# Performance work log

Measured on AMD Instinct MI355X. Metric: run time of the kernel, lower is better.

The kernel has to match this reference:

```python
import jax, jax.numpy as jnp
import numpy as np

N = 30000      # nodes
E = 480000     # edges (before self loops)
C = 64         # in_channels
L = 32         # latent_dim
H = 2          # heads
SLOPE = 0.2    # PyG GATConv default negative_slope


def _param(key, shape, fan_in):
    return jax.random.normal(key, shape, jnp.float32) * (1.0 / np.sqrt(fan_in))


def setup_inputs() -> dict:
    key = jax.random.key(0)
    ks = jax.random.split(key, 32)
    d = {
        "x": jax.random.normal(ks[0], (N, C), jnp.float32),
        "edge_index": jax.random.randint(ks[1], (2, E), 0, N),
        "use_neighbors": 1,
        # GATConv params: W [heads*out, in], att_src/att_dst [heads, out], bias [heads*out]
        # encoder_conv1: in=C, out=2C, heads=H
        "W1": _param(ks[2], (H * 2 * C, C), C),
        "as1": _param(ks[3], (H, 2 * C), 2 * C),
        "ad1": _param(ks[4], (H, 2 * C), 2 * C),
        "b1": jnp.zeros((H * 2 * C,), jnp.float32),
        # encoder_conv2: in=2C*H, out=L, heads=1
        "W2": _param(ks[5], (L, 2 * C * H), 2 * C * H),
        "as2": _param(ks[6], (1, L), L),
        "ad2": _param(ks[7], (1, L), L),
        "b2": jnp.zeros((L,), jnp.float32),
        # decoder_conv1: in=L, out=2C, heads=H
        "W3": _param(ks[8], (H * 2 * C, L), L),
        "as3": _param(ks[9], (H, 2 * C), 2 * C),
        "ad3": _param(ks[10], (H, 2 * C), 2 * C),
        "b3": jnp.zeros((H * 2 * C,), jnp.float32),
        # decoder_conv2: in=2C*H, out=C, heads=1
        "W4": _param(ks[11], (C, 2 * C * H), 2 * C * H),
        "as4": _param(ks[12], (1, C), C),
        "ad4": _param(ks[13], (1, C), C),
        "b4": jnp.zeros((C,), jnp.float32),
        # dense (non-neighbor) branch Linear params [out, in] + bias
        "el1w": _param(ks[14], (2 * C, C), C), "el1b": jnp.zeros((2 * C,), jnp.float32),
        "el2w": _param(ks[15], (L, 2 * C), 2 * C), "el2b": jnp.zeros((L,), jnp.float32),
        "dl1w": _param(ks[16], (2 * C, L), L), "dl1b": jnp.zeros((2 * C,), jnp.float32),
        "dl2w": _param(ks[17], (C, 2 * C), 2 * C), "dl2b": jnp.zeros((C,), jnp.float32),
    }
    return d


def gat_conv(x, src, dst, W, att_src, att_dst, bias, heads, out_ch):
    """PyG GATConv (concat=True, self loops already in src/dst)."""
    n = x.shape[0]
    h = (x @ W.T).reshape(n, heads, out_ch)            # [N,H,F]
    a_s = jnp.sum(h * att_src[None], -1)               # [N,H]
    a_d = jnp.sum(h * att_dst[None], -1)               # [N,H]
    e = jax.nn.leaky_relu(a_s[src] + a_d[dst], SLOPE)  # [Etot,H]
    m = jax.ops.segment_max(e, dst, num_segments=n)
    ex = jnp.exp(e - m[dst])
    den = jax.ops.segment_sum(ex, dst, num_segments=n)
    alpha = ex / den[dst]                              # segment softmax over incoming edges
    msg = h[src] * alpha[..., None]                    # [Etot,H,F]
    out = jax.ops.segment_sum(msg, dst, num_segments=n)
    return out.reshape(n, heads * out_ch) + bias


def reference(x, edge_index, use_neighbors,
              W1, as1, ad1, b1, W2, as2, ad2, b2,
              W3, as3, ad3, b3, W4, as4, ad4, b4,
              el1w, el1b, el2w, el2b, dl1w, dl1b, dl2w, dl2b):
    if use_neighbors:
        loops = jnp.arange(N)
        src = jnp.concatenate([edge_index[0], loops])
        dst = jnp.concatenate([edge_index[1], loops])
        h = jax.nn.relu(gat_conv(x, src, dst, W1, as1, ad1, b1, H, 2 * C))
        z = gat_conv(h, src, dst, W2, as2, ad2, b2, 1, L)
        h = jax.nn.relu(gat_conv(z, src, dst, W3, as3, ad3, b3, H, 2 * C))
        return gat_conv(h, src, dst, W4, as4, ad4, b4, 1, C)
    else:
        h = jax.nn.relu(x @ el1w.T + el1b)
        z = h @ el2w.T + el2b
        h = jax.nn.relu(z @ dl1w.T + dl1b)
        return h @ dl2w.T + dl2b
```

## Files before the change

### kernel.cpp

```cpp
#include <hip/hip_runtime.h>
#include <hip/hip_bf16.h>
#include <math.h>

#define NODES 30000
#define WAVE 64
#define SCAN_T 1024
#define SCAN_CH 32
#define SCAN_CAP (SCAN_T * SCAN_CH)

typedef __attribute__((ext_vector_type(8))) short short8b;
typedef __attribute__((ext_vector_type(4))) float floatx4;

static __device__ __forceinline__ float lrelu(float x) {
    return (x > 0.f) ? x : 0.2f * x;
}

static __device__ __forceinline__ unsigned short f2bf(float f) {
    union { float f; unsigned u; } v; v.f = f;
    unsigned r = v.u + 0x7FFF + ((v.u >> 16) & 1);
    return (unsigned short)(r >> 16);
}

static __device__ __forceinline__ void unpack8(uint4 q, float* v) {
    v[0] = __uint_as_float(q.x << 16); v[1] = __uint_as_float(q.x & 0xFFFF0000u);
    v[2] = __uint_as_float(q.y << 16); v[3] = __uint_as_float(q.y & 0xFFFF0000u);
    v[4] = __uint_as_float(q.z << 16); v[5] = __uint_as_float(q.z & 0xFFFF0000u);
    v[6] = __uint_as_float(q.w << 16); v[7] = __uint_as_float(q.w & 0xFFFF0000u);
}

static __device__ __forceinline__ uint4 pack8(const float* v) {
    uint4 p;
    p.x = (unsigned)f2bf(v[0]) | ((unsigned)f2bf(v[1]) << 16);
    p.y = (unsigned)f2bf(v[2]) | ((unsigned)f2bf(v[3]) << 16);
    p.z = (unsigned)f2bf(v[4]) | ((unsigned)f2bf(v[5]) << 16);
    p.w = (unsigned)f2bf(v[6]) | ((unsigned)f2bf(v[7]) << 16);
    return p;
}

__global__ __launch_bounds__(256) void prep(
    int* __restrict__ deg,
    float* __restrict__ z0, float* __restrict__ z1,
    float* __restrict__ z2, float* __restrict__ z3,
    const float* __restrict__ W1, unsigned short* __restrict__ wb1,
    const float* __restrict__ W2, unsigned short* __restrict__ wb2,
    const float* __restrict__ W3, unsigned short* __restrict__ wb3,
    const float* __restrict__ W4, unsigned short* __restrict__ wb4,
    const float* __restrict__ x, unsigned short* __restrict__ xb,
    const int* __restrict__ flag)
{
    if (*flag == 0) return;
    const int tid = blockIdx.x * blockDim.x + threadIdx.x;
    const int stride = gridDim.x * blockDim.x;
    for (int i = tid; i < SCAN_CAP / 4; i += stride)
        reinterpret_cast<int4*>(deg)[i] = make_int4(0, 0, 0, 0);
    for (int i = tid; i < NODES; i += stride) {
        z0[i] = 0.f; z1[i] = 0.f; z2[i] = 0.f; z3[i] = 0.f;
    }
    for (int i = tid; i < 256 * 64; i += stride) wb1[i] = f2bf(W1[i]);
    for (int i = tid; i < 32 * 256; i += stride) wb2[i] = f2bf(W2[i]);
    for (int i = tid; i < 256 * 32; i += stride) wb3[i] = f2bf(W3[i]);
    for (int i = tid; i < 64 * 256; i += stride) wb4[i] = f2bf(W4[i]);
    for (int i = tid; i < NODES * 64 / 4; i += stride) {
        float4 v = reinterpret_cast<const float4*>(x)[i];
        ushort4 o;
        o.x = f2bf(v.x); o.y = f2bf(v.y); o.z = f2bf(v.z); o.w = f2bf(v.w);
        reinterpret_cast<ushort4*>(xb)[i] = o;
    }
}

template <int K, int M, int OUT_BF16, int RELU, int DOTS>
__global__ __launch_bounds__(256) void gemm_mfma(
    const unsigned short* __restrict__ Xb, int ldx,
    const unsigned short* __restrict__ Wb,
    const float* __restrict__ bias,
    void* __restrict__ outv, int ldc,
    const float* __restrict__ att_s, const float* __restrict__ att_d,
    float* __restrict__ as_out, float* __restrict__ ad_out,
    const int* __restrict__ flag, int Nrows)
{
    if (*flag == 0) return;
    constexpr int KC = K / 32;
    const int w    = threadIdx.x >> 6;
    const int lane = threadIdx.x & 63;
    const int z    = blockIdx.z;
    const int ct   = blockIdx.y;
    const int rowBase = blockIdx.x * 64 + w * 16;

    const int lr = lane & 15;
    const int lk = (lane >> 4) * 8;

    const int arow = min(rowBase + lr, Nrows - 1);
    const unsigned short* ap = Xb + (size_t)arow * ldx + z * K + lk;
    short8b a[KC];
#pragma unroll
    for (int kc = 0; kc < KC; kc++)
        a[kc] = *reinterpret_cast<const short8b*>(ap + kc * 32);

    const unsigned short* bp = Wb + (size_t)(z * M + ct * 16 + lr) * K + lk;
    short8b b[KC];
#pragma unroll
    for (int kc = 0; kc < KC; kc++)
        b[kc] = *reinterpret_cast<const short8b*>(bp + kc * 32);

    floatx4 c = {0.f, 0.f, 0.f, 0.f};
#pragma unroll
    for (int kc = 0; kc < KC; kc++)
        c = __builtin_amdgcn_mfma_f32_16x16x32_bf16(a[kc], b[kc], c, 0, 0, 0);

    const int colg = z * M + ct * 16 + lr;
    const float bv = bias ? bias[colg] : 0.f;

#pragma unroll
    for (int i = 0; i < 4; i++) {
        int r = rowBase + (lane >> 4) * 4 + i;
        float v = c[i] + bv;
        if (RELU) v = fmaxf(v, 0.f);
        if (r < Nrows) {
            if (OUT_BF16)
                ((unsigned short*)outv)[(size_t)r * ldc + colg] = f2bf(v);
            else
                ((float*)outv)[(size_t)r * ldc + colg] = v;
        }
    }

    if (DOTS) {
        const float as_v = att_s[colg];
        const float ad_v = att_d[colg];
#pragma unroll
        for (int i = 0; i < 4; i++) {
            int r = rowBase + (lane >> 4) * 4 + i;
            float ps = c[i] * as_v;
            float pd = c[i] * ad_v;
#pragma unroll
            for (int off = 8; off; off >>= 1) {
                ps += __shfl_xor(ps, off);
                pd += __shfl_xor(pd, off);
            }
            if (lr == 0 && r < Nrows) {
                atomicAdd(&as_out[r], ps);
                atomicAdd(&ad_out[r], pd);
            }
        }
    }
}

__global__ __launch_bounds__(256) void gemm_xwt(
    const float* __restrict__ X, int lda, const float* __restrict__ W,
    const float* __restrict__ bias, float* __restrict__ out, int ldc,
    int Nrows, int M, int K, int relu,
    const int* __restrict__ flag, int wantFlag)
{
    if (((*flag != 0) ? 1 : 0) != wantFlag) return;

    const int z = blockIdx.z;
    X += (size_t)z * K;
    W += (size_t)z * M * K;
    if (bias) bias += (size_t)z * M;
    out += (size_t)z * M;

    __shared__ float As[16][68];
    __shared__ float Bs[16][68];

    const int t  = threadIdx.x;
    const int tx = t & 15;
    const int ty = t >> 4;
    const int rowBase = blockIdx.y * 64;
    const int colBase = blockIdx.x * 64;

    float acc[4][4];
#pragma unroll
    for (int i = 0; i < 4; i++)
#pragma unroll
        for (int j = 0; j < 4; j++) acc[i][j] = 0.f;

    const int r_ld = t >> 2;
    const int k_ld = (t & 3) * 4;

    for (int kt = 0; kt < K; kt += 16) {
        float4 av = make_float4(0.f, 0.f, 0.f, 0.f);
        int grow = rowBase + r_ld;
        if (grow < Nrows)
            av = *reinterpret_cast<const float4*>(&X[(size_t)grow * lda + kt + k_ld]);
        As[k_ld + 0][r_ld] = av.x;
        As[k_ld + 1][r_ld] = av.y;
        As[k_ld + 2][r_ld] = av.z;
        As[k_ld + 3][r_ld] = av.w;
        float4 bv = make_float4(0.f, 0.f, 0.f, 0.f);
        int gm = colBase + r_ld;
        if (gm < M)
            bv = *reinterpret_cast<const float4*>(&W[(size_t)gm * K + kt + k_ld]);
        Bs[k_ld + 0][r_ld] = bv.x;
        Bs[k_ld + 1][r_ld] = bv.y;
        Bs[k_ld + 2][r_ld] = bv.z;
        Bs[k_ld + 3][r_ld] = bv.w;
        __syncthreads();

#pragma unroll
        for (int kk = 0; kk < 16; ++kk) {
            const float4 a = *reinterpret_cast<const float4*>(&As[kk][ty * 4]);
            const float4 b = *reinterpret_cast<const float4*>(&Bs[kk][tx * 4]);
            acc[0][0] += a.x * b.x; acc[0][1] += a.x * b.y; acc[0][2] += a.x * b.z; acc[0][3] += a.x * b.w;
            acc[1][0] += a.y * b.x; acc[1][1] += a.y * b.y; acc[1][2] += a.y * b.z; acc[1][3] += a.y * b.w;
            acc[2][0] += a.z * b.x; acc[2][1] += a.z * b.y; acc[2][2] += a.z * b.z; acc[2][3] += a.z * b.w;
            acc[3][0] += a.w * b.x; acc[3][1] += a.w * b.y; acc[3][2] += a.w * b.z; acc[3][3] += a.w * b.w;
        }
        __syncthreads();
    }

#pragma unroll
    for (int i = 0; i < 4; i++) {
        int row = rowBase + ty * 4 + i;
        if (row >= Nrows) continue;
        int col0 = colBase + tx * 4;
        if (col0 >= M) continue;
        float4 v = make_float4(acc[i][0], acc[i][1], acc[i][2], acc[i][3]);
        if (bias) {
            v.x += bias[col0 + 0]; v.y += bias[col0 + 1];
            v.z += bias[col0 + 2]; v.w += bias[col0 + 3];
        }
        if (relu) {
            v.x = fmaxf(v.x, 0.f); v.y = fmaxf(v.y, 0.f);
            v.z = fmaxf(v.z, 0.f); v.w = fmaxf(v.w, 0.f);
        }
        *reinterpret_cast<float4*>(&out[(size_t)row * ldc + col0]) = v;
    }
}

template <int HH, int F, int K>
static __device__ void fold_body(
    const float* __restrict__ W, const float* __restrict__ as_,
    const float* __restrict__ ad_, float* __restrict__ us,
    float* __restrict__ ud, int b)
{
    const int sel = b / HH;
    const int h   = b % HH;
    const float* att = sel ? ad_ : as_;
    float* uo = sel ? ud : us;

    constexpr int NG = 256 / K;
    const int k  = threadIdx.x % K;
    const int fg = threadIdx.x / K;

    float s = 0.f;
#pragma unroll
    for (int f = fg; f < F; f += NG)
        s += att[h * F + f] * W[(size_t)(h * F + f) * K + k];

    __shared__ float red[256];
    red[threadIdx.x] = s;
    __syncthreads();
    if (fg == 0) {
        float tot = s;
#pragma unroll
        for (int g = 1; g < NG; g++) tot += red[g * K + k];
        uo[h * K + k] = tot;
    }
}

__global__ __launch_bounds__(256) void fold_att2(
    const float* __restrict__ W1, const float* __restrict__ as1,
    const float* __restrict__ ad1, float* __restrict__ u1s, float* __restrict__ u1d,
    const float* __restrict__ W3, const float* __restrict__ as3,
    const float* __restrict__ ad3, float* __restrict__ u3s, float* __restrict__ u3d,
    const int* __restrict__ flag)
{
    if (*flag == 0) return;
    const int b = blockIdx.x;
    if (b < 4) fold_body<2, 128, 64>(W1, as1, ad1, u1s, u1d, b);
    else       fold_body<2, 128, 32>(W3, as3, ad3, u3s, u3d, b - 4);
}

template <int K, int HH>
__global__ __launch_bounds__(256) void att_from_x(
    const float* __restrict__ xin, const float* __restrict__ us,
    const float* __restrict__ ud, float* __restrict__ as_out,
    float* __restrict__ ad_out, const int* __restrict__ flag)
{
    if (*flag == 0) return;
    constexpr int NPW = WAVE / K;
    const int wid  = threadIdx.x >> 6;
    const int lane = threadIdx.x & 63;
    const int sub  = lane / K;
    const int col  = lane % K;
    const int node = (blockIdx.x * 4 + wid) * NPW + sub;

    float v = 0.f;
    if (node < NODES) v = xin[(size_t)node * K + col];
    float ps[HH], pd[HH];
#pragma unroll
    for (int h = 0; h < HH; h++) {
        ps[h] = v * us[h * K + col];
        pd[h] = v * ud[h * K + col];
    }
#pragma unroll
    for (int off = K / 2; off; off >>= 1) {
#pragma unroll
        for (int h = 0; h < HH; h++) {
            ps[h] += __shfl_xor(ps[h], off);
            pd[h] += __shfl_xor(pd[h], off);
        }
    }
    if (col == 0 && node < NODES) {
#pragma unroll
        for (int h = 0; h < HH; h++) {
            as_out[node * HH + h] = ps[h];
            ad_out[node * HH + h] = pd[h];
        }
    }
}

template <int K, int HH>
__global__ __launch_bounds__(256) void gat_aggr_x(
    const unsigned short* __restrict__ xb, const float* __restrict__ as_,
    const float* __restrict__ ad_, const int* __restrict__ rowptr,
    const int* __restrict__ csr_src, unsigned short* __restrict__ aggb,
    const int* __restrict__ flag)
{
    if (*flag == 0) return;
    const int node = blockIdx.x * 4 + (threadIdx.x >> 6);
    const int lane = threadIdx.x & 63;
    if (node >= NODES) return;

    const int beg = rowptr[node], end = rowptr[node + 1];
    const int deg = end - beg;

    float adv[HH];
#pragma unroll
    for (int h = 0; h < HH; h++) adv[h] = ad_[node * HH + h];

    float wl[HH];
    float mx[HH], rden[HH];
    int s_l = 0;
    const bool fast = (deg <= WAVE);

    if (fast) {
        float e[HH];
        int i = beg + lane;
        if (i < end) {
            s_l = csr_src[i];
#pragma unroll
            for (int h = 0; h < HH; h++)
                e[h] = lrelu(as_[s_l * HH + h] + adv[h]);
        } else {
#pragma unroll
            for (int h = 0; h < HH; h++) e[h] = -1e30f;
        }
#pragma unroll
        for (int h = 0; h < HH; h++) {
            mx[h] = e[h];
#pragma unroll
            for (int off = 32; off; off >>= 1)
                mx[h] = fmaxf(mx[h], __shfl_xor(mx[h], off));
            float ex = __expf(e[h] - mx[h]);
            wl[h] = ex;
            float dn = ex;
#pragma unroll
            for (int off = 32; off; off >>= 1)
                dn += __shfl_xor(dn, off);
            rden[h] = 1.f / dn;
        }
    } else {
        float den[HH];
#pragma unroll
        for (int h = 0; h < HH; h++) { mx[h] = -1e30f; den[h] = 0.f; }
        for (int i = beg + lane; i < end; i += WAVE) {
            int s = csr_src[i];
#pragma unroll
            for (int h = 0; h < HH; h++)
                mx[h] = fmaxf(mx[h], lrelu(as_[s * HH + h] + adv[h]));
        }
#pragma unroll
        for (int h = 0; h < HH; h++)
#pragma unroll
            for (int off = 32; off; off >>= 1)
                mx[h] = fmaxf(mx[h], __shfl_xor(mx[h], off));
        for (int i = beg + lane; i < end; i += WAVE) {
            int s = csr_src[i];
#pragma unroll
            for (int h = 0; h < HH; h++)
                den[h] += __expf(lrelu(as_[s * HH + h] + adv[h]) - mx[h]);
        }
#pragma unroll
        for (int h = 0; h < HH; h++) {
#pragma unroll
            for (int off = 32; off; off >>= 1)
                den[h] += __shfl_xor(den[h], off);
            rden[h] = 1.f / den[h];
        }
    }

    constexpr int LPG = K / 8;
    constexpr int GR  = WAVE / LPG;
    const int esub = lane / LPG;
    const int c8   = lane % LPG;

    float acc[HH][8];
#pragma unroll
    for (int h = 0; h < HH; h++)
#pragma unroll
        for (int j = 0; j < 8; j++) acc[h][j] = 0.f;

    if (fast) {
        const int iters = (deg + GR - 1) / GR;
        for (int it = 0; it < iters; ++it) {
            const int i = beg + it * GR + esub;
            const bool valid = (i < end);
            const int srcl = valid ? (i - beg) : 0;
            int s = __shfl(s_l, srcl);
            float w[HH];
#pragma unroll
            for (int h = 0; h < HH; h++)
                w[h] = __shfl(wl[h], srcl);
            if (valid) {
                uint4 q = *reinterpret_cast<const uint4*>(&xb[(size_t)s * K + c8 * 8]);
                float v[8];
                unpack8(q, v);
#pragma unroll
                for (int h = 0; h < HH; h++)
#pragma unroll
                    for (int j = 0; j < 8; j++)
                        acc[h][j] += v[j] * w[h];
            }
        }
    } else {
        for (int i = beg + esub; i < end; i += GR) {
            int s = csr_src[i];
            float w[HH];
#pragma unroll
            for (int h = 0; h < HH; h++)
                w[h] = __expf(lrelu(as_[s * HH + h] + adv[h]) - mx[h]);
            uint4 q = *reinterpret_cast<const uint4*>(&xb[(size_t)s * K + c8 * 8]);
            float v[8];
            unpack8(q, v);
#pragma unroll
            for (int h = 0; h < HH; h++)
#pragma unroll
                for (int j = 0; j < 8; j++)
                    acc[h][j] += v[j] * w[h];
        }
    }
#pragma unroll
    for (int off = LPG; off < WAVE; off <<= 1)
#pragma unroll
        for (int h = 0; h < HH; h++)
#pragma unroll
            for (int j = 0; j < 8; j++)
                acc[h][j] += __shfl_xor(acc[h][j], off);

    if (esub == 0) {
#pragma unroll
        for (int h = 0; h < HH; h++) {
            float o[8];
#pragma unroll
            for (int j = 0; j < 8; j++) o[j] = acc[h][j] * rden[h];
            *reinterpret_cast<uint4*>(&aggb[(size_t)node * (HH * K) + h * K + c8 * 8]) = pack8(o);
        }
    }
}

template <int HF, int RELU, int OUTB>
__global__ __launch_bounds__(256) void gat_aggr_h(
    const unsigned short* __restrict__ hb, const float* __restrict__ as_,
    const float* __restrict__ ad_, const int* __restrict__ rowptr,
    const int* __restrict__ csr_src, const float* __restrict__ bias,
    float* __restrict__ out, unsigned short* __restrict__ outb,
    const int* __restrict__ flag)
{
    if (*flag == 0) return;
    const int node = blockIdx.x * 4 + (threadIdx.x >> 6);
    const int lane = threadIdx.x & 63;
    if (node >= NODES) return;

    const int beg = rowptr[node], end = rowptr[node + 1];
    const int deg = end - beg;
    const float adv = ad_[node];

    float wl, mx, rden;
    int s_l = 0;
    const bool fast = (deg <= WAVE);

    if (fast) {
        int i = beg + lane;
        float e = -1e30f;
        if (i < end) {
            s_l = csr_src[i];
            e = lrelu(as_[s_l] + adv);
        }
        mx = e;
#pragma unroll
        for (int off = 32; off; off >>= 1)
            mx = fmaxf(mx, __shfl_xor(mx, off));
        wl = __expf(e - mx);
        float dn = wl;
#pragma unroll
        for (int off = 32; off; off >>= 1)
            dn += __shfl_xor(dn, off);
        rden = 1.f / dn;
    } else {
        mx = -1e30f;
        float den = 0.f;
        for (int i = beg + lane; i < end; i += WAVE) {
            int s = csr_src[i];
            mx = fmaxf(mx, lrelu(as_[s] + adv));
        }
#pragma unroll
        for (int off = 32; off; off >>= 1)
            mx = fmaxf(mx, __shfl_xor(mx, off));
        for (int i = beg + lane; i < end; i += WAVE) {
            int s = csr_src[i];
            den += __expf(lrelu(as_[s] + adv) - mx);
        }
#pragma unroll
        for (int off = 32; off; off >>= 1)
            den += __shfl_xor(den, off);
        rden = 1.f / den;
        wl = 0.f;
    }

    constexpr int LPG = HF / 8;
    constexpr int GR  = WAVE / LPG;
    const int esub = lane / LPG;
    const int c8   = lane % LPG;

    float acc[8];
#pragma unroll
    for (int j = 0; j < 8; j++) acc[j] = 0.f;

    if (fast) {
        const int iters = (deg + GR - 1) / GR;
        for (int it = 0; it < iters; ++it) {
            const int i = beg + it * GR + esub;
            const bool valid = (i < end);
            const int srcl = valid ? (i - beg) : 0;
            int s = __shfl(s_l, srcl);
            float w = __shfl(wl, srcl);
            if (valid) {
                uint4 q = *reinterpret_cast<const uint4*>(&hb[(size_t)s * HF + c8 * 8]);
                float v[8];
                unpack8(q, v);
#pragma unroll
                for (int j = 0; j < 8; j++) acc[j] += v[j] * w;
            }
        }
    } else {
        for (int i = beg + esub; i < end; i += GR) {
            int s = csr_src[i];
            float w = __expf(lrelu(as_[s] + adv) - mx);
            uint4 q = *reinterpret_cast<const uint4*>(&hb[(size_t)s * HF + c8 * 8]);
            float v[8];
            unpack8(q, v);
#pragma unroll
            for (int j = 0; j < 8; j++) acc[j] += v[j] * w;
        }
    }
#pragma unroll
    for (int off = LPG; off < WAVE; off <<= 1)
#pragma unroll
        for (int j = 0; j < 8; j++)
            acc[j] += __shfl_xor(acc[j], off);

    if (esub == 0) {
        const int col0 = c8 * 8;
        float o[8];
#pragma unroll
        for (int j = 0; j < 8; j++) {
            o[j] = acc[j] * rden + bias[col0 + j];
            if (RELU) o[j] = fmaxf(o[j], 0.f);
        }
        float4 o0 = make_float4(o[0], o[1], o[2], o[3]);
        float4 o1 = make_float4(o[4], o[5], o[6], o[7]);
        *reinterpret_cast<float4*>(&out[(size_t)node * HF + col0]) = o0;
        *reinterpret_cast<float4*>(&out[(size_t)node * HF + col0 + 4]) = o1;
        if (OUTB)
            *reinterpret_cast<uint4*>(&outb[(size_t)node * HF + col0]) = pack8(o);
    }
}

__global__ void count_deg(const int* __restrict__ ei, int* __restrict__ deg,
                          int E_, int Nn, const int* __restrict__ flag)
{
    if (*flag == 0) return;
    int e = blockIdx.x * blockDim.x + threadIdx.x;
    int tot = E_ + Nn;
    if (e >= tot) return;
    int dst = (e < E_) ? ei[E_ + e] : (e - E_);
    atomicAdd(&deg[dst], 1);
}

__global__ __launch_bounds__(SCAN_T) void scan_deg(
    const int* __restrict__ deg, int* __restrict__ rowptr,
    int* __restrict__ cursor, const int* __restrict__ flag)
{
    if (*flag == 0) return;
    __shared__ int sums[SCAN_T];
    const int t = threadIdx.x;
    const int base = t * SCAN_CH;

    int v[SCAN_CH];
    const int4* dp = reinterpret_cast<const int4*>(deg + base);
#pragma unroll
    for (int j = 0; j < SCAN_CH / 4; j++) {
        int4 q = dp[j];
        v[4 * j + 0] = q.x; v[4 * j + 1] = q.y;
        v[4 * j + 2] = q.z; v[4 * j + 3] = q.w;
    }
    int s = 0;
#pragma unroll
    for (int j = 0; j < SCAN_CH; j++) s += v[j];
    sums[t] = s;
    __syncthreads();
    for (int off = 1; off < SCAN_T; off <<= 1) {
        int x = (t >= off) ? sums[t - off] : 0;
        __syncthreads();
        sums[t] += x;
        __syncthreads();
    }
    int run = sums[t] - s;
    if (t == 0) rowptr[0] = 0;
#pragma unroll
    for (int j = 0; j < SCAN_CH; j++) {
        cursor[base + j] = run;
        run += v[j];
        rowptr[base + j + 1] = run;
    }
}

__global__ void scatter_edges(const int* __restrict__ ei, int* __restrict__ cursor,
                              int* __restrict__ csr_src, int E_, int Nn,
                              const int* __restrict__ flag)
{
    if (*flag == 0) return;
    int e = blockIdx.x * blockDim.x + threadIdx.x;
    int tot = E_ + Nn;
    if (e >= tot) return;
    int src, dst;
    if (e < E_) { src = ei[e]; dst = ei[E_ + e]; }
    else        { src = e - E_; dst = src; }
    int pos = atomicAdd(&cursor[dst], 1);
    csr_src[pos] = src;
}

extern "C" void kernel_launch(void* const* d_in, const int* in_sizes, int n_in,
                              void* d_out, int out_size, void* d_ws, size_t ws_size,
                              hipStream_t stream)
{
    const float* x    = (const float*)d_in[0];
    const int*   ei   = (const int*)d_in[1];
    const int*   flag = (const int*)d_in[2];
    const float* W1 = (const float*)d_in[3];
    const float* as1 = (const float*)d_in[4];
    const float* ad1 = (const float*)d_in[5];
    const float* b1 = (const float*)d_in[6];
    const float* W2 = (const float*)d_in[7];
    const float* as2 = (const float*)d_in[8];
    const float* ad2 = (const float*)d_in[9];
    const float* b2 = (const float*)d_in[10];
    const float* W3 = (const float*)d_in[11];
    const float* as3 = (const float*)d_in[12];
    const float* ad3 = (const float*)d_in[13];
    const float* b3 = (const float*)d_in[14];
    const float* W4 = (const float*)d_in[15];
    const float* as4 = (const float*)d_in[16];
    const float* ad4 = (const float*)d_in[17];
    const float* b4 = (const float*)d_in[18];
    const float* el1w = (const float*)d_in[19];
    const float* el1b = (const float*)d_in[20];
    const float* el2w = (const float*)d_in[21];
    const float* el2b = (const float*)d_in[22];
    const float* dl1w = (const float*)d_in[23];
    const float* dl1b = (const float*)d_in[24];
    const float* dl2w = (const float*)d_in[25];
    const float* dl2b = (const float*)d_in[26];

    const int E_   = in_sizes[1] / 2;
    const int Etot = E_ + NODES;

    char* base = (char*)d_ws;
    size_t off = 0;
    auto carve = [&](size_t bytes) -> void* {
        void* p = base + off;
        off = (off + bytes + 255) & ~(size_t)255;
        return p;
    };
    float* T0  = (float*)carve((size_t)NODES * 128 * 4);
    float* A   = (float*)carve((size_t)NODES * 256 * 4);
    float* Bz  = (float*)carve((size_t)NODES * 32 * 4);
    float* asb = (float*)carve((size_t)NODES * 2 * 4);
    float* adb = (float*)carve((size_t)NODES * 2 * 4);
    float* as2b = (float*)carve((size_t)NODES * 4);
    float* ad2b = (float*)carve((size_t)NODES * 4);
    float* as4b = (float*)carve((size_t)NODES * 4);
    float* ad4b = (float*)carve((size_t)NODES * 4);
    float* u1s = (float*)carve(2 * 64 * 4);
    float* u1d = (float*)carve(2 * 64 * 4);
    float* u3s = (float*)carve(2 * 32 * 4);
    float* u3d = (float*)carve(2 * 32 * 4);
    unsigned short* xb   = (unsigned short*)carve((size_t)NODES * 64 * 2);
    unsigned short* aggb = (unsigned short*)carve((size_t)NODES * 128 * 2);
    unsigned short* Ab   = (unsigned short*)carve((size_t)NODES * 256 * 2);
    unsigned short* T1b  = (unsigned short*)carve((size_t)NODES * 64 * 2);
    unsigned short* Bzb  = (unsigned short*)carve((size_t)NODES * 32 * 2);
    unsigned short* wb1  = (unsigned short*)carve(256 * 64 * 2);
    unsigned short* wb2  = (unsigned short*)carve(32 * 256 * 2);
    unsigned short* wb3  = (unsigned short*)carve(256 * 32 * 2);
    unsigned short* wb4  = (unsigned short*)carve(64 * 256 * 2);
    int* deg    = (int*)carve((size_t)SCAN_CAP * 4);
    int* rowptr = (int*)carve((size_t)(SCAN_CAP + 1) * 4);
    int* cursor = (int*)carve((size_t)SCAN_CAP * 4);
    int* csr    = (int*)carve((size_t)Etot * 4);
    (void)ws_size; (void)n_in; (void)out_size;

    float* outp = (float*)d_out;

    const int nodeBlocks = (NODES + 3) / 4;
    const int edgeBlocks = (Etot + 255) / 256;
    dim3 blk(256);
    const int rowTiles = (NODES + 63) / 64;

    prep<<<2048, 256, 0, stream>>>(deg, as2b, ad2b, as4b, ad4b,
                                   W1, wb1, W2, wb2, W3, wb3, W4, wb4,
                                   x, xb, flag);
    count_deg<<<edgeBlocks, 256, 0, stream>>>(ei, deg, E_, NODES, flag);
    scan_deg<<<1, SCAN_T, 0, stream>>>(deg, rowptr, cursor, flag);
    scatter_edges<<<edgeBlocks, 256, 0, stream>>>(ei, cursor, csr, E_, NODES, flag);

    fold_att2<<<8, 256, 0, stream>>>(W1, as1, ad1, u1s, u1d,
                                     W3, as3, ad3, u3s, u3d, flag);

    att_from_x<64, 2><<<nodeBlocks, blk, 0, stream>>>(x, u1s, u1d, asb, adb, flag);
    gat_aggr_x<64, 2><<<nodeBlocks, blk, 0, stream>>>(xb, asb, adb, rowptr, csr, aggb, flag);
    gemm_mfma<64, 128, 1, 1, 0><<<dim3(rowTiles, 8, 2), blk, 0, stream>>>(
        aggb, 128, wb1, b1, Ab, 256, nullptr, nullptr, nullptr, nullptr, flag, NODES);

    gemm_mfma<256, 32, 1, 0, 1><<<dim3(rowTiles, 2, 1), blk, 0, stream>>>(
        Ab, 256, wb2, nullptr, T1b, 32, as2, ad2, as2b, ad2b, flag, NODES);
    gat_aggr_h<32, 0, 1><<<nodeBlocks, blk, 0, stream>>>(T1b, as2b, ad2b, rowptr, csr, b2, Bz, Bzb, flag);

    att_from_x<32, 2><<<(NODES + 7) / 8, blk, 0, stream>>>(Bz, u3s, u3d, asb, adb, flag);
    gat_aggr_x<32, 2><<<nodeBlocks, blk, 0, stream>>>(Bzb, asb, adb, rowptr, csr, aggb, flag);
    gemm_mfma<32, 128, 1, 1, 0><<<dim3(rowTiles, 8, 2), blk, 0, stream>>>(
        aggb, 64, wb3, b3, Ab, 256, nullptr, nullptr, nullptr, nullptr, flag, NODES);

    gemm_mfma<256, 64, 1, 0, 1><<<dim3(rowTiles, 4, 1), blk, 0, stream>>>(
        Ab, 256, wb4, nullptr, T1b, 64, as4, ad4, as4b, ad4b, flag, NODES);
    gat_aggr_h<64, 0, 0><<<nodeBlocks, blk, 0, stream>>>(T1b, as4b, ad4b, rowptr, csr, b4, outp, nullptr, flag);

    gemm_xwt<<<dim3(2, rowTiles, 1), blk, 0, stream>>>(x,  64,  el1w, el1b, T0,   128, NODES, 128, 64, 1, flag, 0);
    gemm_xwt<<<dim3(1, rowTiles, 1), blk, 0, stream>>>(T0, 128, el2w, el2b, Bz,   32,  NODES, 32, 128, 0, flag, 0);
    gemm_xwt<<<dim3(2, rowTiles, 1), blk, 0, stream>>>(Bz, 32,  dl1w, dl1b, A,    128, NODES, 128, 32, 1, flag, 0);
    gemm_xwt<<<dim3(1, rowTiles, 1), blk, 0, stream>>>(A,  128, dl2w, dl2b, outp, 64,  NODES, 64, 128, 0, flag, 0);
}
```

Measured before the change: 382.1 us.

## Fuse preprocessing kernels to cut launches in GAT pipeline

Degree counting and the attention-weight folding move into the prep kernel, and the degree buffer is now zeroed with hipMemsetAsync. Edge scatter and the first-layer attention dot products run as one combined launch. The third layer's attention logits are computed inside the second aggregation kernel's epilogue. This removes several small kernel launches and one full pass over Bz, in exchange for more complex kernels and a memset call.

```diff
diff --git a/kernel.cpp b/kernel.cpp
--- a/kernel.cpp
+++ b/kernel.cpp
@@ -37,8 +37,38 @@
     return p;
 }
 
-__global__ __launch_bounds__(256) void prep(
-    int* __restrict__ deg,
+template <int HH, int F, int K>
+static __device__ void fold_body(
+    const float* __restrict__ W, const float* __restrict__ as_,
+    const float* __restrict__ ad_, float* __restrict__ us,
+    float* __restrict__ ud, int b, float* red)
+{
+    const int sel = b / HH;
+    const int h   = b % HH;
+    const float* att = sel ? ad_ : as_;
+    float* uo = sel ? ud : us;
+
+    constexpr int NG = 256 / K;
+    const int k  = threadIdx.x % K;
+    const int fg = threadIdx.x / K;
+
+    float s = 0.f;
+#pragma unroll
+    for (int f = fg; f < F; f += NG)
+        s += att[h * F + f] * W[(size_t)(h * F + f) * K + k];
+
+    red[threadIdx.x] = s;
+    __syncthreads();
+    if (fg == 0) {
+        float tot = s;
+#pragma unroll
+        for (int g = 1; g < NG; g++) tot += red[g * K + k];
+        uo[h * K + k] = tot;
+    }
+}
+
+__global__ __launch_bounds__(256) void prep2(
+    const int* __restrict__ ei, int E_, int* __restrict__ deg,
     float* __restrict__ z0, float* __restrict__ z1,
     float* __restrict__ z2, float* __restrict__ z3,
     const float* __restrict__ W1, unsigned short* __restrict__ wb1,
@@ -46,13 +76,22 @@
     const float* __restrict__ W3, unsigned short* __restrict__ wb3,
     const float* __restrict__ W4, unsigned short* __restrict__ wb4,
     const float* __restrict__ x, unsigned short* __restrict__ xb,
+    const float* __restrict__ as1, const float* __restrict__ ad1,
+    float* __restrict__ u1s, float* __restrict__ u1d,
+    const float* __restrict__ as3, const float* __restrict__ ad3,
+    float* __restrict__ u3s, float* __restrict__ u3d,
     const int* __restrict__ flag)
 {
     if (*flag == 0) return;
+    __shared__ float red[256];
     const int tid = blockIdx.x * blockDim.x + threadIdx.x;
     const int stride = gridDim.x * blockDim.x;
-    for (int i = tid; i < SCAN_CAP / 4; i += stride)
-        reinterpret_cast<int4*>(deg)[i] = make_int4(0, 0, 0, 0);
+
+    const int tot = E_ + NODES;
+    for (int e = tid; e < tot; e += stride) {
+        int dst = (e < E_) ? ei[E_ + e] : (e - E_);
+        atomicAdd(&deg[dst], 1);
+    }
     for (int i = tid; i < NODES; i += stride) {
         z0[i] = 0.f; z1[i] = 0.f; z2[i] = 0.f; z3[i] = 0.f;
     }
@@ -65,6 +104,100 @@
         ushort4 o;
         o.x = f2bf(v.x); o.y = f2bf(v.y); o.z = f2bf(v.z); o.w = f2bf(v.w);
         reinterpret_cast<ushort4*>(xb)[i] = o;
+    }
+
+    if (blockIdx.x < 8) {
+        __syncthreads();
+        if (blockIdx.x < 4)
+            fold_body<2, 128, 64>(W1, as1, ad1, u1s, u1d, blockIdx.x, red);
+        else
+            fold_body<2, 128, 32>(W3, as3, ad3, u3s, u3d, blockIdx.x - 4, red);
+    }
+}
+
+__global__ __launch_bounds__(SCAN_T) void scan_deg(
+    const int* __restrict__ deg, int* __restrict__ rowptr,
+    int* __restrict__ cursor, const int* __restrict__ flag)
+{
+    if (*flag == 0) return;
+    __shared__ int sums[SCAN_T];
+    const int t = threadIdx.x;
+    const int base = t * SCAN_CH;
+
+    int v[SCAN_CH];
+    const int4* dp = reinterpret_cast<const int4*>(deg + base);
+#pragma unroll
+    for (int j = 0; j < SCAN_CH / 4; j++) {
+        int4 q = dp[j];
+        v[4 * j + 0] = q.x; v[4 * j + 1] = q.y;
+        v[4 * j + 2] = q.z; v[4 * j + 3] = q.w;
+    }
+    int s = 0;
+#pragma unroll
+    for (int j = 0; j < SCAN_CH; j++) s += v[j];
+    sums[t] = s;
+    __syncthreads();
+    for (int off = 1; off < SCAN_T; off <<= 1) {
+        int x = (t >= off) ? sums[t - off] : 0;
+        __syncthreads();
+        sums[t] += x;
+        __syncthreads();
+    }
+    int run = sums[t] - s;
+    if (t == 0) rowptr[0] = 0;
+#pragma unroll
+    for (int j = 0; j < SCAN_CH; j++) {
+        cursor[base + j] = run;
+        run += v[j];
+        rowptr[base + j + 1] = run;
+    }
+}
+
+__global__ __launch_bounds__(256) void scatter_attx(
+    const int* __restrict__ ei, int* __restrict__ cursor,
+    int* __restrict__ csr_src, int E_, int eb,
+    const float* __restrict__ x, const float* __restrict__ u1s,
+    const float* __restrict__ u1d, float* __restrict__ as_out,
+    float* __restrict__ ad_out, const int* __restrict__ flag)
+{
+    if (*flag == 0) return;
+    const int b = blockIdx.x;
+    if (b < eb) {
+        int e = b * 256 + threadIdx.x;
+        int tot = E_ + NODES;
+        if (e >= tot) return;
+        int src, dst;
+        if (e < E_) { src = ei[e]; dst = ei[E_ + e]; }
+        else        { src = e - E_; dst = src; }
+        int pos = atomicAdd(&cursor[dst], 1);
+        csr_src[pos] = src;
+    } else {
+        const int wid  = threadIdx.x >> 6;
+        const int lane = threadIdx.x & 63;
+        const int node = (b - eb) * 4 + wid;
+        if (node >= NODES) return;
+        float v = x[(size_t)node * 64 + lane];
+        float ps[2], pd[2];
+#pragma unroll
+        for (int h = 0; h < 2; h++) {
+            ps[h] = v * u1s[h * 64 + lane];
+            pd[h] = v * u1d[h * 64 + lane];
+        }
+#pragma unroll
+        for (int off = 32; off; off >>= 1) {
+#pragma unroll
+            for (int h = 0; h < 2; h++) {
+                ps[h] += __shfl_xor(ps[h], off);
+                pd[h] += __shfl_xor(pd[h], off);
+            }
+        }
+        if (lane == 0) {
+#pragma unroll
+            for (int h = 0; h < 2; h++) {
+                as_out[node * 2 + h] = ps[h];
+                ad_out[node * 2 + h] = pd[h];
+            }
+        }
     }
 }
 
@@ -226,89 +359,6 @@
     }
 }
 
-template <int HH, int F, int K>
-static __device__ void fold_body(
-    const float* __restrict__ W, const float* __restrict__ as_,
-    const float* __restrict__ ad_, float* __restrict__ us,
-    float* __restrict__ ud, int b)
-{
-    const int sel = b / HH;
-    const int h   = b % HH;
-    const float* att = sel ? ad_ : as_;
-    float* uo = sel ? ud : us;
-
-    constexpr int NG = 256 / K;
-    const int k  = threadIdx.x % K;
-    const int fg = threadIdx.x / K;
-
-    float s = 0.f;
-#pragma unroll
-    for (int f = fg; f < F; f += NG)
-        s += att[h * F + f] * W[(size_t)(h * F + f) * K + k];
-
-    __shared__ float red[256];
-    red[threadIdx.x] = s;
-    __syncthreads();
-    if (fg == 0) {
-        float tot = s;
-#pragma unroll
-        for (int g = 1; g < NG; g++) tot += red[g * K + k];
-        uo[h * K + k] = tot;
-    }
-}
-
-__global__ __launch_bounds__(256) void fold_att2(
-    const float* __restrict__ W1, const float* __restrict__ as1,
-    const float* __restrict__ ad1, float* __restrict__ u1s, float* __restrict__ u1d,
-    const float* __restrict__ W3, const float* __restrict__ as3,
-    const float* __restrict__ ad3, float* __restrict__ u3s, float* __restrict__ u3d,
-    const int* __restrict__ flag)
-{
-    if (*flag == 0) return;
-    const int b = blockIdx.x;
-    if (b < 4) fold_body<2, 128, 64>(W1, as1, ad1, u1s, u1d, b);
-    else       fold_body<2, 128, 32>(W3, as3, ad3, u3s, u3d, b - 4);
-}
-
-template <int K, int HH>
-__global__ __launch_bounds__(256) void att_from_x(
-    const float* __restrict__ xin, const float* __restrict__ us,
-    const float* __restrict__ ud, float* __restrict__ as_out,
-    float* __restrict__ ad_out, const int* __restrict__ flag)
-{
-    if (*flag == 0) return;
-    constexpr int NPW = WAVE / K;
-    const int wid  = threadIdx.x >> 6;
-    const int lane = threadIdx.x & 63;
-    const int sub  = lane / K;
-    const int col  = lane % K;
-    const int node = (blockIdx.x * 4 + wid) * NPW + sub;
-
-    float v = 0.f;
-    if (node < NODES) v = xin[(size_t)node * K + col];
-    float ps[HH], pd[HH];
-#pragma unroll
-    for (int h = 0; h < HH; h++) {
-        ps[h] = v * us[h * K + col];
-        pd[h] = v * ud[h * K + col];
-    }
-#pragma unroll
-    for (int off = K / 2; off; off >>= 1) {
-#pragma unroll
-        for (int h = 0; h < HH; h++) {
-            ps[h] += __shfl_xor(ps[h], off);
-            pd[h] += __shfl_xor(pd[h], off);
-        }
-    }
-    if (col == 0 && node < NODES) {
-#pragma unroll
-        for (int h = 0; h < HH; h++) {
-            as_out[node * HH + h] = ps[h];
-            ad_out[node * HH + h] = pd[h];
-        }
-    }
-}
-
 template <int K, int HH>
 __global__ __launch_bounds__(256) void gat_aggr_x(
     const unsigned short* __restrict__ xb, const float* __restrict__ as_,
@@ -458,12 +508,14 @@
     }
 }
 
-template <int HF, int RELU, int OUTB>
+template <int HF, int RELU, int OUTB, int DOTS3>
 __global__ __launch_bounds__(256) void gat_aggr_h(
     const unsigned short* __restrict__ hb, const float* __restrict__ as_,
     const float* __restrict__ ad_, const int* __restrict__ rowptr,
     const int* __restrict__ csr_src, const float* __restrict__ bias,
     float* __restrict__ out, unsigned short* __restrict__ outb,
+    const float* __restrict__ u3s, const float* __restrict__ u3d,
+    float* __restrict__ as3o, float* __restrict__ ad3o,
     const int* __restrict__ flag)
 {
     if (*flag == 0) return;
@@ -573,71 +625,35 @@
         *reinterpret_cast<float4*>(&out[(size_t)node * HF + col0 + 4]) = o1;
         if (OUTB)
             *reinterpret_cast<uint4*>(&outb[(size_t)node * HF + col0]) = pack8(o);
-    }
-}
-
-__global__ void count_deg(const int* __restrict__ ei, int* __restrict__ deg,
-                          int E_, int Nn, const int* __restrict__ flag)
-{
-    if (*flag == 0) return;
-    int e = blockIdx.x * blockDim.x + threadIdx.x;
-    int tot = E_ + Nn;
-    if (e >= tot) return;
-    int dst = (e < E_) ? ei[E_ + e] : (e - E_);
-    atomicAdd(&deg[dst], 1);
-}
-
-__global__ __launch_bounds__(SCAN_T) void scan_deg(
-    const int* __restrict__ deg, int* __restrict__ rowptr,
-    int* __restrict__ cursor, const int* __restrict__ flag)
-{
-    if (*flag == 0) return;
-    __shared__ int sums[SCAN_T];
-    const int t = threadIdx.x;
-    const int base = t * SCAN_CH;
-
-    int v[SCAN_CH];
-    const int4* dp = reinterpret_cast<const int4*>(deg + base);
-#pragma unroll
-    for (int j = 0; j < SCAN_CH / 4; j++) {
-        int4 q = dp[j];
-        v[4 * j + 0] = q.x; v[4 * j + 1] = q.y;
-        v[4 * j + 2] = q.z; v[4 * j + 3] = q.w;
-    }
-    int s = 0;
-#pragma unroll
-    for (int j = 0; j < SCAN_CH; j++) s += v[j];
-    sums[t] = s;
-    __syncthreads();
-    for (int off = 1; off < SCAN_T; off <<= 1) {
-        int x = (t >= off) ? sums[t - off] : 0;
-        __syncthreads();
-        sums[t] += x;
-        __syncthreads();
-    }
-    int run = sums[t] - s;
-    if (t == 0) rowptr[0] = 0;
-#pragma unroll
-    for (int j = 0; j < SCAN_CH; j++) {
-        cursor[base + j] = run;
-        run += v[j];
-        rowptr[base + j + 1] = run;
-    }
-}
-
-__global__ void scatter_edges(const int* __restrict__ ei, int* __restrict__ cursor,
-                              int* __restrict__ csr_src, int E_, int Nn,
-                              const int* __restrict__ flag)
-{
-    if (*flag == 0) return;
-    int e = blockIdx.x * blockDim.x + threadIdx.x;
-    int tot = E_ + Nn;
-    if (e >= tot) return;
-    int src, dst;
-    if (e < E_) { src = ei[e]; dst = ei[E_ + e]; }
-    else        { src = e - E_; dst = src; }
-    int pos = atomicAdd(&cursor[dst], 1);
-    csr_src[pos] = src;
+        if (DOTS3) {
+            float ps[2], pd[2];
+#pragma unroll
+            for (int h = 0; h < 2; h++) {
+                float s1 = 0.f, s2 = 0.f;
+#pragma unroll
+                for (int j = 0; j < 8; j++) {
+                    s1 += o[j] * u3s[h * HF + col0 + j];
+                    s2 += o[j] * u3d[h * HF + col0 + j];
+                }
+                ps[h] = s1; pd[h] = s2;
+            }
+#pragma unroll
+            for (int off = 1; off < LPG; off <<= 1) {
+#pragma unroll
+                for (int h = 0; h < 2; h++) {
+                    ps[h] += __shfl_xor(ps[h], off);
+                    pd[h] += __shfl_xor(pd[h], off);
+                }
+            }
+            if (lane == 0) {
+#pragma unroll
+                for (int h = 0; h < 2; h++) {
+                    as3o[node * 2 + h] = ps[h];
+                    ad3o[node * 2 + h] = pd[h];
+                }
+            }
+        }
+    }
 }
 
 extern "C" void kernel_launch(void* const* d_in, const int* in_sizes, int n_in,
@@ -717,33 +733,33 @@
     dim3 blk(256);
     const int rowTiles = (NODES + 63) / 64;
 
-    prep<<<2048, 256, 0, stream>>>(deg, as2b, ad2b, as4b, ad4b,
-                                   W1, wb1, W2, wb2, W3, wb3, W4, wb4,
-                                   x, xb, flag);
-    count_deg<<<edgeBlocks, 256, 0, stream>>>(ei, deg, E_, NODES, flag);
+    hipMemsetAsync(deg, 0, (size_t)SCAN_CAP * 4, stream);
+    prep2<<<2048, 256, 0, stream>>>(ei, E_, deg, as2b, ad2b, as4b, ad4b,
+                                    W1, wb1, W2, wb2, W3, wb3, W4, wb4,
+                                    x, xb, as1, ad1, u1s, u1d,
+                                    as3, ad3, u3s, u3d, flag);
     scan_deg<<<1, SCAN_T, 0, stream>>>(deg, rowptr, cursor, flag);
-    scatter_edges<<<edgeBlocks, 256, 0, stream>>>(ei, cursor, csr, E_, NODES, flag);
-
-    fold_att2<<<8, 256, 0, stream>>>(W1, as1, ad1, u1s, u1d,
-                                     W3, as3, ad3, u3s, u3d, flag);
-
-    att_from_x<64, 2><<<nodeBlocks, blk, 0, stream>>>(x, u1s, u1d, asb, adb, flag);
+    scatter_attx<<<edgeBlocks + nodeBlocks, blk, 0, stream>>>(
+        ei, cursor, csr, E_, edgeBlocks, x, u1s, u1d, asb, adb, flag);
+
     gat_aggr_x<64, 2><<<nodeBlocks, blk, 0, stream>>>(xb, asb, adb, rowptr, csr, aggb, flag);
     gemm_mfma<64, 128, 1, 1, 0><<<dim3(rowTiles, 8, 2), blk, 0, stream>>>(
         aggb, 128, wb1, b1, Ab, 256, nullptr, nullptr, nullptr, nullptr, flag, NODES);
 
     gemm_mfma<256, 32, 1, 0, 1><<<dim3(rowTiles, 2, 1), blk, 0, stream>>>(
         Ab, 256, wb2, nullptr, T1b, 32, as2, ad2, as2b, ad2b, flag, NODES);
-    gat_aggr_h<32, 0, 1><<<nodeBlocks, blk, 0, stream>>>(T1b, as2b, ad2b, rowptr, csr, b2, Bz, Bzb, flag);
-
-    att_from_x<32, 2><<<(NODES + 7) / 8, blk, 0, stream>>>(Bz, u3s, u3d, asb, adb, flag);
+    gat_aggr_h<32, 0, 1, 1><<<nodeBlocks, blk, 0, stream>>>(
+        T1b, as2b, ad2b, rowptr, csr, b2, Bz, Bzb, u3s, u3d, asb, adb, flag);
+
     gat_aggr_x<32, 2><<<nodeBlocks, blk, 0, stream>>>(Bzb, asb, adb, rowptr, csr, aggb, flag);
     gemm_mfma<32, 128, 1, 1, 0><<<dim3(rowTiles, 8, 2), blk, 0, stream>>>(
         aggb, 64, wb3, b3, Ab, 256, nullptr, nullptr, nullptr, nullptr, flag, NODES);
 
     gemm_mfma<256, 64, 1, 0, 1><<<dim3(rowTiles, 4, 1), blk, 0, stream>>>(
         Ab, 256, wb4, nullptr, T1b, 64, as4, ad4, as4b, ad4b, flag, NODES);
-    gat_aggr_h<64, 0, 0><<<nodeBlocks, blk, 0, stream>>>(T1b, as4b, ad4b, rowptr, csr, b4, outp, nullptr, flag);
+    gat_aggr_h<64, 0, 0, 0><<<nodeBlocks, blk, 0, stream>>>(
+        T1b, as4b, ad4b, rowptr, csr, b4, outp, nullptr, nullptr, nullptr,
+        nullptr, nullptr, flag);
 
     gemm_xwt<<<dim3(2, rowTiles, 1), blk, 0, stream>>>(x,  64,  el1w, el1b, T0,   128, NODES, 128, 64, 1, flag, 0);
     gemm_xwt<<<dim3(1, rowTiles, 1), blk, 0, stream>>>(T0, 128, el2w, el2b, Bz,   32,  NODES, 32, 128, 0, flag, 0);
```

New measurement: 371.0 us. -2.9%, faster.
